# Performance work log

Hardware: AMD Instinct MI355X
Metric: run time of the kernel (lower is better)

Reference implementation:

```python
import jax, jax.numpy as jnp
import numpy as np


def setup_inputs() -> dict:
    key = jax.random.key(0)
    ks = jax.random.split(key, 7)
    N, D, K = 500000, 128, 32
    return {
        "x": jax.random.normal(ks[0], (N, D), dtype=jnp.float32),
        "h_e": jax.random.normal(ks[1], (N, D), dtype=jnp.float32),
        "bond_n": jax.random.uniform(ks[2], (K, N), dtype=jnp.float32),
        "W_i_w": jax.random.normal(ks[3], (D, 2 * D), dtype=jnp.float32) * 0.05,
        "W_i_b": jax.random.normal(ks[4], (D,), dtype=jnp.float32) * 0.05,
        "W_m_w": jax.random.normal(ks[5], (D, D), dtype=jnp.float32) * 0.05,
        "W_m_b": jax.random.normal(ks[6], (D,), dtype=jnp.float32) * 0.05,
    }


def reference(x, h_e, bond_n, W_i_w, W_i_b, W_m_w, W_m_b):
    # h_n = relu(W_i([x ; h_e]))  -> [N, D]
    h_n = jax.nn.relu(jnp.concatenate([x, h_e], axis=1) @ W_i_w.T + W_i_b)
    # m = sum_k sum_n bond_n[k,n] * h_n[n,:]  -> [D]
    # (equivalent to torch: (bond_n[...,None] * h_n).sum(1).sum(0),
    #  but expressed as a contraction to avoid the [K,N,D] intermediate)
    m = jnp.einsum('kn,nd->d', bond_n, h_n)
    # h = relu(h_n + W_m(m))  -> [N, D] via broadcast of the [D] message
    h = jax.nn.relu(h_n + (m @ W_m_w.T + W_m_b))
    return h
```

## Files before the change

### kernel.cpp

```cpp
#include <hip/hip_runtime.h>
#include <stdint.h>
#include <stddef.h>

#define N_ROWS 500000
#define DDIM   128
#define K2     256
#define KBOND  32
#define TILE   16
#define NTL    (N_ROWS / TILE)
#define NBLK   768
#define MR_BLKS 12
#define P2_BLOCKS 2048

typedef float  f32x4  __attribute__((ext_vector_type(4)));
typedef __bf16 bf16x8 __attribute__((ext_vector_type(8)));
typedef __bf16 bf16x4 __attribute__((ext_vector_type(4)));

__device__ __bf16 g_wbf[DDIM * K2];
__device__ float  g_s[N_ROWS];
__device__ float  g_partials[NBLK * DDIM];
__device__ float  g_p2[MR_BLKS * DDIM];
__device__ float  g_msg[DDIM];
__device__ __bf16 g_hn[(size_t)N_ROWS * DDIM];

__global__ void k_prep(const float* __restrict__ w) {
  int t = blockIdx.x * blockDim.x + threadIdx.x;
  if (t < DDIM * K2) g_wbf[t] = (__bf16)w[t];
}

__global__ __launch_bounds__(256)
void k_s(const float* __restrict__ bond) {
  int n = blockIdx.x * 256 + threadIdx.x;
  if (n >= N_ROWS) return;
  float a = 0.f, b = 0.f;
  #pragma unroll
  for (int k = 0; k < KBOND; k += 2) {
    a += bond[(size_t)k * N_ROWS + n];
    b += bond[(size_t)(k + 1) * N_ROWS + n];
  }
  g_s[n] = a + b;
}

__global__ __launch_bounds__(256, 3)
void k_pass1(const float* __restrict__ x, const float* __restrict__ he,
             const float* __restrict__ bias)
{
  __shared__ __align__(16) unsigned char a_lds[2][TILE * 512];

  const int tid  = threadIdx.x;
  const int w    = tid >> 6;
  const int lane = tid & 63;
  const int l15  = lane & 15;
  const int g    = lane >> 4;

  bf16x8 wfrag[2][8];
  #pragma unroll
  for (int dg = 0; dg < 2; ++dg)
    #pragma unroll
    for (int ks = 0; ks < 8; ++ks)
      wfrag[dg][ks] = *(const bf16x8*)(g_wbf +
          (size_t)(32 * w + 16 * dg + l15) * K2 + 32 * ks + 8 * g);

  f32x4 bv0 = *(const f32x4*)(bias + 32 * w + 4 * g);
  f32x4 bv1 = *(const f32x4*)(bias + 32 * w + 16 + 4 * g);

  const int sr = tid >> 4;
  const int sc = tid & 15;
  const unsigned swz   = (unsigned)(sr << 4);
  const unsigned wo_x  = (unsigned)(sr * 512) + ((16u * sc) ^ swz);
  const unsigned wo_he = (unsigned)(sr * 512) + ((256u + 16u * sc) ^ swz);
  const unsigned rsw   = (unsigned)(l15 << 4);

  f32x4 macc0 = (f32x4)(0.f), macc1 = (f32x4)(0.f);
  int t = blockIdx.x;

  {
    const float* xr = x  + (size_t)(t * TILE + sr) * DDIM + 8 * sc;
    const float* hr = he + (size_t)(t * TILE + sr) * DDIM + 8 * sc;
    f32x4 xa = *(const f32x4*)xr, xb = *(const f32x4*)(xr + 4);
    f32x4 ha = *(const f32x4*)hr, hb = *(const f32x4*)(hr + 4);
    bf16x8 bx, bh;
    #pragma unroll
    for (int i = 0; i < 4; ++i) {
      bx[i] = (__bf16)xa[i]; bx[4 + i] = (__bf16)xb[i];
      bh[i] = (__bf16)ha[i]; bh[4 + i] = (__bf16)hb[i];
    }
    *(bf16x8*)(&a_lds[0][wo_x])  = bx;
    *(bf16x8*)(&a_lds[0][wo_he]) = bh;
  }
  float s0 = g_s[t * TILE + l15];
  __builtin_amdgcn_sched_barrier(0);
  asm volatile("s_waitcnt lgkmcnt(0)");
  __builtin_amdgcn_s_barrier();
  __builtin_amdgcn_sched_barrier(0);

  int cur = 0;
  while (true) {
    const int  tn  = t + NBLK;
    const bool has = tn < NTL;
    const int  tl  = has ? tn : t;

    const float* xr = x  + (size_t)(tl * TILE + sr) * DDIM + 8 * sc;
    const float* hr = he + (size_t)(tl * TILE + sr) * DDIM + 8 * sc;
    f32x4 xa = *(const f32x4*)xr, xb = *(const f32x4*)(xr + 4);
    f32x4 ha = *(const f32x4*)hr, hb = *(const f32x4*)(hr + 4);
    float s0n = g_s[tl * TILE + l15];
    __builtin_amdgcn_sched_barrier(0);

    f32x4 acc0 = (f32x4)(0.f), acc1 = (f32x4)(0.f);
    const unsigned char* base = &a_lds[cur][0];
    #pragma unroll
    for (int ks = 0; ks < 8; ++ks) {
      const unsigned o = (unsigned)(64 * ks + 16 * g);
      bf16x8 b = *(const bf16x8*)(base + l15 * 512 + (o ^ rsw));
      acc0 = __builtin_amdgcn_mfma_f32_16x16x32_bf16(wfrag[0][ks], b, acc0, 0, 0, 0);
      acc1 = __builtin_amdgcn_mfma_f32_16x16x32_bf16(wfrag[1][ks], b, acc1, 0, 0, 0);
    }

    {
      const int n = t * TILE + l15;
      f32x4 h0, h1;
      #pragma unroll
      for (int i = 0; i < 4; ++i) {
        float a = acc0[i] + bv0[i]; h0[i] = a > 0.f ? a : 0.f;
        float b = acc1[i] + bv1[i]; h1[i] = b > 0.f ? b : 0.f;
      }
      #pragma unroll
      for (int i = 0; i < 4; ++i) { macc0[i] += s0 * h0[i]; macc1[i] += s0 * h1[i]; }
      bf16x4 hb0, hb1;
      #pragma unroll
      for (int i = 0; i < 4; ++i) { hb0[i] = (__bf16)h0[i]; hb1[i] = (__bf16)h1[i]; }
      *(bf16x4*)(g_hn + (size_t)n * DDIM + 32 * w + 4 * g)      = hb0;
      *(bf16x4*)(g_hn + (size_t)n * DDIM + 32 * w + 16 + 4 * g) = hb1;
    }
    __builtin_amdgcn_sched_barrier(0);

    {
      bf16x8 bx, bh;
      #pragma unroll
      for (int i = 0; i < 4; ++i) {
        bx[i] = (__bf16)xa[i]; bx[4 + i] = (__bf16)xb[i];
        bh[i] = (__bf16)ha[i]; bh[4 + i] = (__bf16)hb[i];
      }
      *(bf16x8*)(&a_lds[cur ^ 1][wo_x])  = bx;
      *(bf16x8*)(&a_lds[cur ^ 1][wo_he]) = bh;
    }
    __builtin_amdgcn_sched_barrier(0);
    asm volatile("s_waitcnt lgkmcnt(0)");
    __builtin_amdgcn_s_barrier();
    __builtin_amdgcn_sched_barrier(0);

    if (!has) break;
    t = tn; cur ^= 1; s0 = s0n;
  }

  #pragma unroll
  for (int off = 1; off <= 8; off <<= 1) {
    #pragma unroll
    for (int i = 0; i < 4; ++i) {
      macc0[i] += __shfl_xor(macc0[i], off, 64);
      macc1[i] += __shfl_xor(macc1[i], off, 64);
    }
  }
  if (l15 == 0) {
    *(f32x4*)(&g_partials[(size_t)blockIdx.x * DDIM + 32 * w + 4 * g])      = macc0;
    *(f32x4*)(&g_partials[(size_t)blockIdx.x * DDIM + 32 * w + 16 + 4 * g]) = macc1;
  }
}

__global__ void k_mr() {
  const int d    = threadIdx.x & 127;
  const int half = threadIdx.x >> 7;
  const int r0   = blockIdx.x * 64;
  float acc = 0.f;
  for (int r = r0 + half; r < r0 + 64; r += 2)
    acc += g_partials[(size_t)r * DDIM + d];
  __shared__ float sp[DDIM];
  if (half == 0) sp[d] = acc;
  __syncthreads();
  if (half == 1) g_p2[blockIdx.x * DDIM + d] = sp[d] + acc;
}

__global__ void k_msg(const float* __restrict__ wm, const float* __restrict__ bm) {
  __shared__ float ms[DDIM];
  const int d = threadIdx.x;
  float s = 0.f;
  #pragma unroll
  for (int c = 0; c < MR_BLKS; ++c) s += g_p2[c * DDIM + d];
  ms[d] = s;
  __syncthreads();
  float acc = bm[d];
  #pragma unroll 8
  for (int j = 0; j < DDIM; ++j) acc += ms[j] * wm[(size_t)d * DDIM + j];
  g_msg[d] = acc;
}

__global__ __launch_bounds__(256)
void k_pass2(float* __restrict__ out)
{
  __shared__ float ms[DDIM];
  if (threadIdx.x < DDIM) ms[threadIdx.x] = g_msg[threadIdx.x];
  __syncthreads();
  const size_t total = (size_t)N_ROWS * DDIM / 8;
  for (size_t c = (size_t)blockIdx.x * blockDim.x + threadIdx.x; c < total;
       c += (size_t)gridDim.x * blockDim.x) {
    const size_t base = c * 8;
    const int col0 = (int)(base & (DDIM - 1));
    bf16x8 hv = *(const bf16x8*)(g_hn + base);
    f32x4 o0, o1;
    #pragma unroll
    for (int i = 0; i < 4; ++i) {
      float a = (float)hv[i]     + ms[col0 + i];
      float b = (float)hv[4 + i] + ms[col0 + 4 + i];
      o0[i] = a > 0.f ? a : 0.f;
      o1[i] = b > 0.f ? b : 0.f;
    }
    *(f32x4*)(out + base)     = o0;
    *(f32x4*)(out + base + 4) = o1;
  }
}

extern "C" void kernel_launch(void* const* d_in, const int* in_sizes, int n_in,
                              void* d_out, int out_size, void* d_ws, size_t ws_size,
                              hipStream_t stream) {
  const float* x    = (const float*)d_in[0];
  const float* he   = (const float*)d_in[1];
  const float* bond = (const float*)d_in[2];
  const float* wi   = (const float*)d_in[3];
  const float* bi   = (const float*)d_in[4];
  const float* wm   = (const float*)d_in[5];
  const float* bm   = (const float*)d_in[6];
  float* out = (float*)d_out;
  (void)d_ws; (void)ws_size;

  k_prep<<<(DDIM * K2 + 255) / 256, 256, 0, stream>>>(wi);
  k_s<<<(N_ROWS + 255) / 256, 256, 0, stream>>>(bond);
  k_pass1<<<NBLK, 256, 0, stream>>>(x, he, bi);
  k_mr<<<MR_BLKS, 256, 0, stream>>>();
  k_msg<<<1, 128, 0, stream>>>(wm, bm);
  k_pass2<<<P2_BLOCKS, 256, 0, stream>>>(out);
}
```

Baseline: 264.3 us.

## Deepen pass1 prefetch to two tiles ahead and raise grid occupancy

The main pass1 loop now keeps two register sets of x/h_e/bond-sum data in flight, issuing global loads two tiles ahead instead of one. The loop is unrolled into two alternating phases so the register sets swap roles without copies. The block count rises from 768 to 1024 with launch bounds targeting 4 blocks per SM, and the reduction block count is adjusted to match. This aims to hide global memory latency better in a bandwidth-bound stream, at the cost of extra registers that may cause spilling under the tighter occupancy bound.

Result: slower. 350.5 us (+32.6%).

```diff
diff --git a/kernel.cpp b/kernel.cpp
--- a/kernel.cpp
+++ b/kernel.cpp
@@ -8,8 +8,8 @@
 #define KBOND  32
 #define TILE   16
 #define NTL    (N_ROWS / TILE)
-#define NBLK   768
-#define MR_BLKS 12
+#define NBLK   1024
+#define MR_BLKS 16
 #define P2_BLOCKS 2048
 
 typedef float  f32x4  __attribute__((ext_vector_type(4)));
@@ -41,7 +41,7 @@
   g_s[n] = a + b;
 }
 
-__global__ __launch_bounds__(256, 3)
+__global__ __launch_bounds__(256, 4)
 void k_pass1(const float* __restrict__ x, const float* __restrict__ he,
              const float* __restrict__ bias)
 {
@@ -73,86 +73,107 @@
 
   f32x4 macc0 = (f32x4)(0.f), macc1 = (f32x4)(0.f);
   int t = blockIdx.x;
+  int cur = 0;
+
+  f32x4 xa0, xb0, ha0, hb0;  float sA;
+  f32x4 xa1, xb1, ha1, hb1;  float sB;
 
   {
     const float* xr = x  + (size_t)(t * TILE + sr) * DDIM + 8 * sc;
     const float* hr = he + (size_t)(t * TILE + sr) * DDIM + 8 * sc;
-    f32x4 xa = *(const f32x4*)xr, xb = *(const f32x4*)(xr + 4);
-    f32x4 ha = *(const f32x4*)hr, hb = *(const f32x4*)(hr + 4);
+    xa0 = *(const f32x4*)xr; xb0 = *(const f32x4*)(xr + 4);
+    ha0 = *(const f32x4*)hr; hb0 = *(const f32x4*)(hr + 4);
+    sA  = g_s[t * TILE + l15];
+  }
+  {
+    const int t1 = t + NBLK;
+    const int tl = (t1 < NTL) ? t1 : t;
+    const float* xr = x  + (size_t)(tl * TILE + sr) * DDIM + 8 * sc;
+    const float* hr = he + (size_t)(tl * TILE + sr) * DDIM + 8 * sc;
+    xa1 = *(const f32x4*)xr; xb1 = *(const f32x4*)(xr + 4);
+    ha1 = *(const f32x4*)hr; hb1 = *(const f32x4*)(hr + 4);
+    sB  = g_s[tl * TILE + l15];
+  }
+  {
     bf16x8 bx, bh;
     #pragma unroll
     for (int i = 0; i < 4; ++i) {
-      bx[i] = (__bf16)xa[i]; bx[4 + i] = (__bf16)xb[i];
-      bh[i] = (__bf16)ha[i]; bh[4 + i] = (__bf16)hb[i];
+      bx[i] = (__bf16)xa0[i]; bx[4 + i] = (__bf16)xb0[i];
+      bh[i] = (__bf16)ha0[i]; bh[4 + i] = (__bf16)hb0[i];
     }
     *(bf16x8*)(&a_lds[0][wo_x])  = bx;
     *(bf16x8*)(&a_lds[0][wo_he]) = bh;
   }
-  float s0 = g_s[t * TILE + l15];
   __builtin_amdgcn_sched_barrier(0);
   asm volatile("s_waitcnt lgkmcnt(0)");
   __builtin_amdgcn_s_barrier();
   __builtin_amdgcn_sched_barrier(0);
 
-  int cur = 0;
-  while (true) {
-    const int  tn  = t + NBLK;
-    const bool has = tn < NTL;
-    const int  tl  = has ? tn : t;
-
-    const float* xr = x  + (size_t)(tl * TILE + sr) * DDIM + 8 * sc;
-    const float* hr = he + (size_t)(tl * TILE + sr) * DDIM + 8 * sc;
-    f32x4 xa = *(const f32x4*)xr, xb = *(const f32x4*)(xr + 4);
-    f32x4 ha = *(const f32x4*)hr, hb = *(const f32x4*)(hr + 4);
-    float s0n = g_s[tl * TILE + l15];
-    __builtin_amdgcn_sched_barrier(0);
-
-    f32x4 acc0 = (f32x4)(0.f), acc1 = (f32x4)(0.f);
-    const unsigned char* base = &a_lds[cur][0];
-    #pragma unroll
-    for (int ks = 0; ks < 8; ++ks) {
-      const unsigned o = (unsigned)(64 * ks + 16 * g);
-      bf16x8 b = *(const bf16x8*)(base + l15 * 512 + (o ^ rsw));
-      acc0 = __builtin_amdgcn_mfma_f32_16x16x32_bf16(wfrag[0][ks], b, acc0, 0, 0, 0);
-      acc1 = __builtin_amdgcn_mfma_f32_16x16x32_bf16(wfrag[1][ks], b, acc1, 0, 0, 0);
-    }
-
-    {
-      const int n = t * TILE + l15;
-      f32x4 h0, h1;
-      #pragma unroll
-      for (int i = 0; i < 4; ++i) {
-        float a = acc0[i] + bv0[i]; h0[i] = a > 0.f ? a : 0.f;
-        float b = acc1[i] + bv1[i]; h1[i] = b > 0.f ? b : 0.f;
-      }
-      #pragma unroll
-      for (int i = 0; i < 4; ++i) { macc0[i] += s0 * h0[i]; macc1[i] += s0 * h1[i]; }
-      bf16x4 hb0, hb1;
-      #pragma unroll
-      for (int i = 0; i < 4; ++i) { hb0[i] = (__bf16)h0[i]; hb1[i] = (__bf16)h1[i]; }
-      *(bf16x4*)(g_hn + (size_t)n * DDIM + 32 * w + 4 * g)      = hb0;
-      *(bf16x4*)(g_hn + (size_t)n * DDIM + 32 * w + 16 + 4 * g) = hb1;
-    }
-    __builtin_amdgcn_sched_barrier(0);
-
-    {
-      bf16x8 bx, bh;
-      #pragma unroll
-      for (int i = 0; i < 4; ++i) {
-        bx[i] = (__bf16)xa[i]; bx[4 + i] = (__bf16)xb[i];
-        bh[i] = (__bf16)ha[i]; bh[4 + i] = (__bf16)hb[i];
-      }
-      *(bf16x8*)(&a_lds[cur ^ 1][wo_x])  = bx;
-      *(bf16x8*)(&a_lds[cur ^ 1][wo_he]) = bh;
-    }
-    __builtin_amdgcn_sched_barrier(0);
-    asm volatile("s_waitcnt lgkmcnt(0)");
-    __builtin_amdgcn_s_barrier();
-    __builtin_amdgcn_sched_barrier(0);
-
-    if (!has) break;
-    t = tn; cur ^= 1; s0 = s0n;
-  }
+#define PHASE(LXA,LXB,LHA,LHB,LSN, WXA,WXB,WHA,WHB)                          \
+  do {                                                                       \
+    const float scur_ = LSN;            \
+    const int t2 = t + 2 * NBLK;                                             \
+    const int tl = (t2 < NTL) ? t2 : t;                                      \
+    const float* xr = x  + (size_t)(tl * TILE + sr) * DDIM + 8 * sc;         \
+    const float* hr = he + (size_t)(tl * TILE + sr) * DDIM + 8 * sc;         \
+    LXA = *(const f32x4*)xr; LXB = *(const f32x4*)(xr + 4);                  \
+    LHA = *(const f32x4*)hr; LHB = *(const f32x4*)(hr + 4);                  \
+    LSN = g_s[tl * TILE + l15];                                              \
+    __builtin_amdgcn_sched_barrier(0);                                       \
+    f32x4 acc0 = (f32x4)(0.f), acc1 = (f32x4)(0.f);                          \
+    {                                                                        \
+      const unsigned char* base_ = &a_lds[cur][0];                           \
+      _Pragma("unroll")                                                      \
+      for (int ks = 0; ks < 8; ++ks) {                                       \
+        const unsigned o = (unsigned)(64 * ks + 16 * g);                     \
+        bf16x8 b = *(const bf16x8*)(base_ + l15 * 512 + (o ^ rsw));          \
+        acc0 = __builtin_amdgcn_mfma_f32_16x16x32_bf16(wfrag[0][ks], b, acc0, 0, 0, 0); \
+        acc1 = __builtin_amdgcn_mfma_f32_16x16x32_bf16(wfrag[1][ks], b, acc1, 0, 0, 0); \
+      }                                                                      \
+    }                                                                        \
+    {                                                                        \
+      const int n_ = t * TILE + l15;                                         \
+      f32x4 h0, h1;                                                          \
+      _Pragma("unroll")                                                      \
+      for (int i = 0; i < 4; ++i) {                                          \
+        float a_ = acc0[i] + bv0[i]; h0[i] = a_ > 0.f ? a_ : 0.f;            \
+        float b_ = acc1[i] + bv1[i]; h1[i] = b_ > 0.f ? b_ : 0.f;            \
+      }                                                                      \
+      _Pragma("unroll")                                                      \
+      for (int i = 0; i < 4; ++i) { macc0[i] += scur_ * h0[i];               \
+                                    macc1[i] += scur_ * h1[i]; }             \
+      bf16x4 q0, q1;                                                         \
+      _Pragma("unroll")                                                      \
+      for (int i = 0; i < 4; ++i) { q0[i] = (__bf16)h0[i];                   \
+                                    q1[i] = (__bf16)h1[i]; }                 \
+      *(bf16x4*)(g_hn + (size_t)n_ * DDIM + 32 * w + 4 * g)      = q0;       \
+      *(bf16x4*)(g_hn + (size_t)n_ * DDIM + 32 * w + 16 + 4 * g) = q1;       \
+    }                                                                        \
+    __builtin_amdgcn_sched_barrier(0);                                       \
+    {                                                                        \
+      bf16x8 bx, bh;                                                         \
+      _Pragma("unroll")                                                      \
+      for (int i = 0; i < 4; ++i) {                                          \
+        bx[i] = (__bf16)WXA[i]; bx[4 + i] = (__bf16)WXB[i];                  \
+        bh[i] = (__bf16)WHA[i]; bh[4 + i] = (__bf16)WHB[i];                  \
+      }                                                                      \
+      *(bf16x8*)(&a_lds[cur ^ 1][wo_x])  = bx;                               \
+      *(bf16x8*)(&a_lds[cur ^ 1][wo_he]) = bh;                               \
+    }                                                                        \
+    __builtin_amdgcn_sched_barrier(0);                                       \
+    asm volatile("s_waitcnt lgkmcnt(0)");                                    \
+    __builtin_amdgcn_s_barrier();                                            \
+    __builtin_amdgcn_sched_barrier(0);                                       \
+    cur ^= 1;                                                                \
+  } while (0)
+
+  for (;;) {
+    PHASE(xa0, xb0, ha0, hb0, sA,  xa1, xb1, ha1, hb1);
+    t += NBLK; if (t >= NTL) break;
+    PHASE(xa1, xb1, ha1, hb1, sB,  xa0, xb0, ha0, hb0);
+    t += NBLK; if (t >= NTL) break;
+  }
+#undef PHASE
 
   #pragma unroll
   for (int off = 1; off <= 8; off <<= 1) {
```
